# Kernel tuning notes

Hardware: AMD Instinct MI355X
Metric: run time of the kernel (lower is better)

The kernel has to match this reference:

```python
import jax, jax.numpy as jnp
import numpy as np

BATCH = 512
HIDDEN_DIM = 4096
NUM_CODES = 32
CODE_DIM = 64
CODEBOOK_SIZE = 1024


def _lsa_single(cost):
    """Rectangular Hungarian (Jonker-Volgenant shortest augmenting path).
    cost: [n, m] with n <= m. Returns, for each row, the assigned column,
    minimizing total cost (matches scipy.optimize.linear_sum_assignment)."""
    n, m = cost.shape
    u = np.zeros(n + 1)
    v = np.zeros(m + 1)
    p = np.zeros(m + 1, dtype=np.int64)  # p[j]: row matched to col j (1-based); 0 = free
    for i in range(1, n + 1):
        p[0] = i
        j0 = 0
        minv = np.full(m + 1, np.inf)
        way = np.zeros(m + 1, dtype=np.int64)
        used = np.zeros(m + 1, dtype=bool)
        while True:
            used[j0] = True
            i0 = p[j0]
            free = ~used
            free[0] = False
            jfree = np.nonzero(free)[0]
            cur = cost[i0 - 1, jfree - 1] - u[i0] - v[jfree]
            upd = cur < minv[jfree]
            minv[jfree[upd]] = cur[upd]
            way[jfree[upd]] = j0
            k = jfree[np.argmin(minv[jfree])]
            delta = minv[k]
            u[p[used]] += delta
            v[used] -= delta
            minv[free] -= delta
            j0 = k
            if p[j0] == 0:
                break
        while j0 != 0:  # augment along the path
            j1 = way[j0]
            p[j0] = p[j1]
            j0 = j1
    ans = np.empty(n, dtype=np.int64)
    for j in range(1, m + 1):
        if p[j] > 0:
            ans[p[j] - 1] = j - 1
    return ans


def _lsa_batch(costs):
    costs = np.asarray(costs, dtype=np.float64)
    return np.stack([_lsa_single(c) for c in costs]).astype(np.int32)


def setup_inputs() -> dict:
    key = jax.random.key(0)
    ks = jax.random.split(key, 4)
    return {
        "x": jax.random.normal(ks[0], (BATCH, HIDDEN_DIM), jnp.float32),
        "codebook": jax.random.normal(ks[1], (CODEBOOK_SIZE, CODE_DIM), jnp.float32),
        "enc_w": jax.random.normal(ks[2], (NUM_CODES * CODE_DIM, HIDDEN_DIM), jnp.float32) * 0.02,
        "enc_b": jnp.zeros((NUM_CODES * CODE_DIM,), jnp.float32),
        "dec_w": jax.random.normal(ks[3], (HIDDEN_DIM, NUM_CODES * CODE_DIM), jnp.float32) * 0.02,
        "dec_b": jnp.zeros((HIDDEN_DIM,), jnp.float32),
    }


def reference(x, codebook, enc_w, enc_b, dec_w, dec_b):
    bs = x.shape[0]
    # encoder (torch Linear: y = x @ W.T + b)
    e = (x @ enc_w.T + enc_b).reshape(bs, NUM_CODES, CODE_DIM)
    ef = e.reshape(-1, CODE_DIM)  # [bs*num_codes, code_dim]
    # pairwise Euclidean distances to codebook entries [bs*num_codes, codebook_size]
    d2 = (jnp.sum(ef * ef, axis=1, keepdims=True)
          + jnp.sum(codebook * codebook, axis=1)
          - 2.0 * (ef @ codebook.T))
    dist = jnp.sqrt(jnp.maximum(d2, 0.0)).reshape(bs, NUM_CODES, CODEBOOK_SIZE)
    # per-sample Hungarian assignment (original uses scipy on CPU; sqrt is
    # monotone so the optimal assignment is identical)
    indices = jax.pure_callback(
        _lsa_batch,
        jax.ShapeDtypeStruct((bs, NUM_CODES), jnp.int32),
        jax.lax.stop_gradient(dist),
    )
    flat_idx = indices.reshape(-1)  # matches torch's concatenated flat indices
    q = codebook[flat_idx].reshape(bs, NUM_CODES, CODE_DIM)
    # straight-through estimator
    q_st = e + jax.lax.stop_gradient(q - e)
    r = q_st.reshape(bs, NUM_CODES * CODE_DIM) @ dec_w.T + dec_b
    return (r, q, e, flat_idx)
```

## Files before the change

kernel.cpp:

```cpp
#include <hip/hip_runtime.h>
#include <hip/hip_bf16.h>
#include <stdint.h>

#define BATCH 512
#define HID   4096
#define NC    32
#define CD    64
#define CB    1024
#define NCD   2048

typedef unsigned short u16;
typedef unsigned int   u32;
typedef __attribute__((ext_vector_type(8))) short short8;
typedef __attribute__((ext_vector_type(4))) float f32x4;

#define WAVE_SYNC()  asm volatile("s_waitcnt lgkmcnt(0)" ::: "memory")
#define SCHED_FENCE() __builtin_amdgcn_sched_barrier(0)

__device__ inline u16 bf16_rne(float f) {
  u32 u = __builtin_bit_cast(u32, f);
  u32 r = u + 0x7FFFu + ((u >> 16) & 1u);
  return (u16)(r >> 16);
}
__device__ inline float bf16_f32(u16 h) {
  u32 u = ((u32)h) << 16;
  return __builtin_bit_cast(float, u);
}
__device__ inline void split3(float a, u16& h1, u16& h2, u16& h3) {
  h1 = bf16_rne(a);
  float r1 = a - bf16_f32(h1);
  h2 = bf16_rne(r1);
  float r2 = r1 - bf16_f32(h2);
  h3 = bf16_rne(r2);
}
__device__ inline f32x4 mfma16(short8 a, short8 b, f32x4 c) {
  return __builtin_amdgcn_mfma_f32_16x16x32_bf16(a, b, c, 0, 0, 0);
}
__device__ inline void gload_lds16(const u16* g, u16* l) {
  __builtin_amdgcn_global_load_lds(
      (const __attribute__((address_space(1))) u32*)(const void*)g,
      (__attribute__((address_space(3))) u32*)(void*)l, 16, 0, 0);
}

union H8 { u16 h[8]; short8 v; };

template<int K>
__global__ __launch_bounds__(256) void conv_split3(
    const float* __restrict__ src, u16* __restrict__ d1,
    u16* __restrict__ d2, u16* __restrict__ d3) {
  const int t = threadIdx.x;
  const int g = blockIdx.x * 4 + (t >> 6);
  const int l = t & 63;
  const int n  = (g / (K / 32)) * 16 + (l & 15);
  const int k0 = (g % (K / 32)) * 32 + (l >> 4) * 8;
  const float* s = src + (size_t)n * K + k0;
  H8 o1, o2, o3;
#pragma unroll
  for (int i = 0; i < 8; ++i) split3(s[i], o1.h[i], o2.h[i], o3.h[i]);
  size_t off = (size_t)g * 512 + l * 8;
  *(short8*)(d1 + off) = o1.v;
  *(short8*)(d2 + off) = o2.v;
  *(short8*)(d3 + off) = o3.v;
}

template<int K>
__global__ __launch_bounds__(256) void conv_split1(
    const float* __restrict__ src, u16* __restrict__ d1) {
  const int t = threadIdx.x;
  const int g = blockIdx.x * 4 + (t >> 6);
  const int l = t & 63;
  const int n  = (g / (K / 32)) * 16 + (l & 15);
  const int k0 = (g % (K / 32)) * 32 + (l >> 4) * 8;
  const float* s = src + (size_t)n * K + k0;
  H8 o1;
#pragma unroll
  for (int i = 0; i < 8; ++i) o1.h[i] = bf16_rne(s[i]);
  *(short8*)(d1 + (size_t)g * 512 + l * 8) = o1.v;
}

__global__ __launch_bounds__(512) void k1_gemm(
    const float* __restrict__ A,
    const u16* __restrict__ B1, const u16* __restrict__ B2,
    const u16* __restrict__ B3, float* __restrict__ part) {
  __shared__ u16 As[3][8][64][8];
  __shared__ u16 Bs[3][8][64][8];
  const int t = threadIdx.x;
  const int wid = t >> 6, lane = t & 63;
  const int wrow = wid >> 2, wcol = wid & 3;
  const int bm = blockIdx.x * 128;
  const int bn = blockIdx.y * 128;
  const int kz = blockIdx.z;
  const int kbase = kz * 1024;
  const int arow = t >> 2;
  const int akc  = t & 3;
  const float* aptr = A + (size_t)(bm + arow) * HID + kbase + akc * 8;
  const int arf = arow >> 4, all_ = (akc << 4) | (arow & 15);
  const size_t nf0 = (size_t)((bn >> 4) + wid);

  f32x4 acc[4][2];
#pragma unroll
  for (int r = 0; r < 4; ++r)
#pragma unroll
    for (int c = 0; c < 2; ++c) acc[r][c] = (f32x4)0.f;

  for (int ks = 0; ks < 32; ++ks) {
    float v[8];
    *(f32x4*)&v[0] = *(const f32x4*)(aptr + ks * 32);
    *(f32x4*)&v[4] = *(const f32x4*)(aptr + ks * 32 + 4);
    {
      size_t gb = (nf0 * 128 + (size_t)((kbase >> 5) + ks)) * 512 + lane * 8;
      gload_lds16(B1 + gb, &Bs[0][wid][0][0]);
      gload_lds16(B2 + gb, &Bs[1][wid][0][0]);
      gload_lds16(B3 + gb, &Bs[2][wid][0][0]);
    }
    {
      H8 s1, s2, s3;
#pragma unroll
      for (int i = 0; i < 8; ++i) split3(v[i], s1.h[i], s2.h[i], s3.h[i]);
      *(short8*)&As[0][arf][all_][0] = s1.v;
      *(short8*)&As[1][arf][all_][0] = s2.v;
      *(short8*)&As[2][arf][all_][0] = s3.v;
    }
    __syncthreads();
    short8 a0[4], a1[4], a2[4], b0[2], b1[2], b2[2];
#pragma unroll
    for (int r = 0; r < 4; ++r) {
      a0[r] = *(const short8*)&As[0][wrow * 4 + r][lane][0];
      a1[r] = *(const short8*)&As[1][wrow * 4 + r][lane][0];
      a2[r] = *(const short8*)&As[2][wrow * 4 + r][lane][0];
    }
#pragma unroll
    for (int c = 0; c < 2; ++c) {
      b0[c] = *(const short8*)&Bs[0][wcol * 2 + c][lane][0];
      b1[c] = *(const short8*)&Bs[1][wcol * 2 + c][lane][0];
      b2[c] = *(const short8*)&Bs[2][wcol * 2 + c][lane][0];
    }
#pragma unroll
    for (int r = 0; r < 4; ++r)
#pragma unroll
      for (int c = 0; c < 2; ++c) {
        f32x4 d = acc[r][c];
        d = mfma16(a0[r], b0[c], d);
        d = mfma16(a0[r], b1[c], d);
        d = mfma16(a1[r], b0[c], d);
        d = mfma16(a1[r], b1[c], d);
        d = mfma16(a0[r], b2[c], d);
        d = mfma16(a2[r], b0[c], d);
        acc[r][c] = d;
      }
    __syncthreads();
  }
  float* P = part + (size_t)kz * BATCH * NCD;
#pragma unroll
  for (int r = 0; r < 4; ++r)
#pragma unroll
    for (int c = 0; c < 2; ++c) {
      int row = bm + wrow * 64 + r * 16 + (lane >> 4) * 4;
      int col = bn + wcol * 32 + c * 16 + (lane & 15);
#pragma unroll
      for (int i = 0; i < 4; ++i)
        P[(size_t)(row + i) * NCD + col] = acc[r][c][i];
    }
}

__global__ __launch_bounds__(256) void k_reduce_bias(
    const float* __restrict__ part, const float* __restrict__ bias,
    float* __restrict__ e) {
  size_t o = ((size_t)blockIdx.x * 256 + threadIdx.x) * 4;
  int n = (int)(o & (NCD - 1));
  f32x4 s = *(const f32x4*)(part + o);
  s += *(const f32x4*)(part + (size_t)1 * BATCH * NCD + o);
  s += *(const f32x4*)(part + (size_t)2 * BATCH * NCD + o);
  s += *(const f32x4*)(part + (size_t)3 * BATCH * NCD + o);
  s += *(const f32x4*)(bias + n);
  *(f32x4*)(e + o) = s;
}

__global__ __launch_bounds__(512) void k3_gemm(
    const u16* __restrict__ Ab, const u16* __restrict__ Bb,
    const float* __restrict__ bias, float* __restrict__ C) {
  __shared__ u16 As[4][64][8];
  __shared__ u16 Bs[8][64][8];
  const int t = threadIdx.x;
  const int wid = t >> 6, lane = t & 63;
  const int wrow = wid >> 2, wcol = wid & 3;
  const int bm = blockIdx.x * 64, bn = blockIdx.y * 128;
  f32x4 acc[2][2];
#pragma unroll
  for (int r = 0; r < 2; ++r)
#pragma unroll
    for (int c = 0; c < 2; ++c) acc[r][c] = (f32x4)0.f;

  for (int ks = 0; ks < 64; ++ks) {
    {
      size_t gb = (((size_t)(bn >> 4) + wid) * 64 + ks) * 512 + lane * 8;
      gload_lds16(Bb + gb, &Bs[wid][0][0]);
      if (wid < 4) {
        size_t ga = (((size_t)(bm >> 4) + wid) * 64 + ks) * 512 + lane * 8;
        gload_lds16(Ab + ga, &As[wid][0][0]);
      }
    }
    __syncthreads();
    short8 a[2], b[2];
#pragma unroll
    for (int r = 0; r < 2; ++r) a[r] = *(const short8*)&As[wrow * 2 + r][lane][0];
#pragma unroll
    for (int c = 0; c < 2; ++c) b[c] = *(const short8*)&Bs[wcol * 2 + c][lane][0];
#pragma unroll
    for (int r = 0; r < 2; ++r)
#pragma unroll
      for (int c = 0; c < 2; ++c) acc[r][c] = mfma16(a[r], b[c], acc[r][c]);
    __syncthreads();
  }
#pragma unroll
  for (int r = 0; r < 2; ++r)
#pragma unroll
    for (int c = 0; c < 2; ++c) {
      int row = bm + wrow * 32 + r * 16 + (lane >> 4) * 4;
      int col = bn + wcol * 32 + c * 16 + (lane & 15);
      float bb = bias[col];
#pragma unroll
      for (int i = 0; i < 4; ++i)
        C[(size_t)(row + i) * HID + col] = acc[r][c][i] + bb;
    }
}

__global__ __launch_bounds__(256) void k_cost(
    const float* __restrict__ e_glob, const float* __restrict__ codebook,
    float* __restrict__ cost) {
  __shared__ float es[64][68];
  __shared__ float cs[64][68];
  __shared__ float enorm[64], cnorm[64];
  const int t = threadIdx.x;
  const int r0 = blockIdx.x * 64;
  const int c0 = blockIdx.y * 256;
  const int tx = t & 15, ty = t >> 4;
  {
    int row = t & 63, kq = t >> 6;
    const float* src = e_glob + (size_t)(r0 + row) * 64 + kq * 16;
#pragma unroll
    for (int i = 0; i < 4; ++i) {
      float4 v = *(const float4*)(src + i * 4);
      int kk = kq * 16 + i * 4;
      es[kk + 0][row] = v.x; es[kk + 1][row] = v.y;
      es[kk + 2][row] = v.z; es[kk + 3][row] = v.w;
    }
  }
  __syncthreads();
  if (t < 64) {
    float s = 0.f;
    for (int kk = 0; kk < 64; ++kk) { float x = es[kk][t]; s = fmaf(x, x, s); }
    enorm[t] = s;
  }
  for (int sub = 0; sub < 4; ++sub) {
    __syncthreads();
    {
      int col = t & 63, kq = t >> 6;
      const float* src = codebook + (size_t)(c0 + sub * 64 + col) * 64 + kq * 16;
#pragma unroll
      for (int i = 0; i < 4; ++i) {
        float4 v = *(const float4*)(src + i * 4);
        int kk = kq * 16 + i * 4;
        cs[kk + 0][col] = v.x; cs[kk + 1][col] = v.y;
        cs[kk + 2][col] = v.z; cs[kk + 3][col] = v.w;
      }
    }
    __syncthreads();
    if (t < 64) {
      float s = 0.f;
      for (int kk = 0; kk < 64; ++kk) { float x = cs[kk][t]; s = fmaf(x, x, s); }
      cnorm[t] = s;
    }
    __syncthreads();
    float dot[4][4] = {};
#pragma unroll 8
    for (int kk = 0; kk < 64; ++kk) {
      float4 a4 = *(const float4*)&es[kk][ty * 4];
      float4 b4 = *(const float4*)&cs[kk][tx * 4];
      float a_[4] = {a4.x, a4.y, a4.z, a4.w};
      float b_[4] = {b4.x, b4.y, b4.z, b4.w};
#pragma unroll
      for (int i = 0; i < 4; ++i)
#pragma unroll
        for (int j = 0; j < 4; ++j)
          dot[i][j] = fmaf(a_[i], b_[j], dot[i][j]);
    }
#pragma unroll
    for (int i = 0; i < 4; ++i) {
      int r = ty * 4 + i;
      float en = enorm[r];
      float4 o;
      o.x = sqrtf(fmaxf(en + cnorm[tx * 4 + 0] - 2.f * dot[i][0], 0.f));
      o.y = sqrtf(fmaxf(en + cnorm[tx * 4 + 1] - 2.f * dot[i][1], 0.f));
      o.z = sqrtf(fmaxf(en + cnorm[tx * 4 + 2] - 2.f * dot[i][2], 0.f));
      o.w = sqrtf(fmaxf(en + cnorm[tx * 4 + 3] - 2.f * dot[i][3], 0.f));
      *(float4*)&cost[(size_t)(r0 + r) * CB + c0 + sub * 64 + tx * 4] = o;
    }
  }
}

__global__ __launch_bounds__(64) void k_assign(
    const float* __restrict__ cost_g, const float* __restrict__ codebook,
    float* __restrict__ q_out, float* __restrict__ idx_out) {
  __shared__ int idxl[32];
  const int lane = threadIdx.x;
  const int s = blockIdx.x;
  const float* __restrict__ cost = cost_g + (size_t)s * NC * CB;

  double v_[16], minv_[16];
  u32 way_[16], pm_[16];
  double u_val = 0.0;
#pragma unroll
  for (int r = 0; r < 16; ++r) { v_[r] = 0.0; pm_[r] = 0; }

  float pf[16];
#pragma unroll
  for (int r = 0; r < 16; ++r) pf[r] = cost[r * 64 + lane];

  for (int i = 1; i <= NC; ++i) {
#pragma unroll
    for (int r = 0; r < 16; ++r) minv_[r] = 1e300;
    u32 col_used = 0;
    unsigned long long rowmask = 0ull;
    int j0 = 0;
    int i0 = i;
    int first = 1;
    for (int guard = 0; guard < 1056; ++guard) {
      rowmask |= (1ull << i0);
      const double ui0 = __shfl(u_val, i0);
      float cc[16];
      if (first) {
#pragma unroll
        for (int r = 0; r < 16; ++r) cc[r] = pf[r];
        if (i < NC) {
#pragma unroll
          for (int r = 0; r < 16; ++r)
            pf[r] = cost[(size_t)i * CB + r * 64 + lane];
        }
        first = 0;
      } else {
        const float* crow = cost + (size_t)(i0 - 1) * CB;
#pragma unroll
        for (int r = 0; r < 16; ++r) cc[r] = crow[r * 64 + lane];
      }
      double bv = 1e301; int bj = 1 << 20;
#pragma unroll
      for (int r = 0; r < 16; ++r) {
        const int j = 1 + lane + r * 64;
        if (!((col_used >> r) & 1u)) {
          double cur = (double)cc[r] - ui0 - v_[r];
          if (cur < minv_[r]) { minv_[r] = cur; way_[r] = (u32)j0; }
          if (minv_[r] < bv) { bv = minv_[r]; bj = j; }
        }
      }
#pragma unroll
      for (int off = 1; off < 64; off <<= 1) {
        double ov = __shfl_xor(bv, off);
        int oj = __shfl_xor(bj, off);
        if (ov < bv || (ov == bv && oj < bj)) { bv = ov; bj = oj; }
      }
      const double delta = bv;
      const int k = bj;
      if ((rowmask >> lane) & 1ull) u_val += delta;
#pragma unroll
      for (int r = 0; r < 16; ++r) {
        const int j = 1 + lane + r * 64;
        if ((col_used >> r) & 1u) v_[r] -= delta;
        else {
          minv_[r] -= delta;
          if (j == k) col_used |= (1u << r);
        }
      }
      const int rk = (k - 1) >> 6, kl = (k - 1) & 63;
      u32 sel = 0;
#pragma unroll
      for (int r = 0; r < 16; ++r) if (r == rk) sel = pm_[r];
      const int pmk = __shfl((int)sel, kl);
      j0 = k;
      if (pmk == 0) break;
      i0 = pmk;
    }
    int jj = j0;
    while (jj != 0) {
      const int rj = (jj - 1) >> 6, lj = (jj - 1) & 63;
      u32 wsel = 0;
#pragma unroll
      for (int r = 0; r < 16; ++r) if (r == rj) wsel = way_[r];
      const int j1 = __shfl((int)wsel, lj);
      int newpm;
      if (j1 == 0) newpm = i;
      else {
        const int r1 = (j1 - 1) >> 6, l1 = (j1 - 1) & 63;
        u32 psel = 0;
#pragma unroll
        for (int r = 0; r < 16; ++r) if (r == r1) psel = pm_[r];
        newpm = __shfl((int)psel, l1);
      }
#pragma unroll
      for (int r = 0; r < 16; ++r)
        if (lane == lj && r == rj) pm_[r] = (u32)newpm;
      jj = j1;
    }
  }

#pragma unroll
  for (int r = 0; r < 16; ++r)
    if (pm_[r] > 0) idxl[pm_[r] - 1] = lane + r * 64;
  WAVE_SYNC(); SCHED_FENCE();
  if (lane < NC) idx_out[(size_t)s * NC + lane] = (float)idxl[lane];
#pragma unroll
  for (int p = 0; p < 8; ++p) {
    int vi = p * 64 + lane;
    int r = vi >> 4, c4 = vi & 15;
    int ci = idxl[r];
    float4 qv = *(const float4*)&codebook[(size_t)ci * 64 + c4 * 4];
    *(float4*)&q_out[(size_t)s * NCD + r * 64 + c4 * 4] = qv;
  }
}

extern "C" void kernel_launch(void* const* d_in, const int* in_sizes, int n_in,
                              void* d_out, int out_size, void* d_ws, size_t ws_size,
                              hipStream_t stream) {
  (void)in_sizes; (void)n_in; (void)out_size; (void)ws_size;
  const float* x        = (const float*)d_in[0];
  const float* codebook = (const float*)d_in[1];
  const float* enc_w    = (const float*)d_in[2];
  const float* enc_b    = (const float*)d_in[3];
  const float* dec_w    = (const float*)d_in[4];
  const float* dec_b    = (const float*)d_in[5];

  float* out = (float*)d_out;
  float* r_out   = out;
  float* q_out   = out + 2097152;
  float* e_out   = out + 2097152 + 1048576;
  float* idx_out = out + 2097152 + 2097152;

  char* ws = (char*)d_ws;
  u16* B1 = (u16*)ws;
  u16* B2 = (u16*)(ws + (16u << 20));
  u16* B3 = (u16*)(ws + (32u << 20));
  float* part = (float*)(ws + (48u << 20));
  float* cost_ws = (float*)ws;
  u16* qb  = (u16*)ws;
  u16* dwb = (u16*)(ws + (2u << 20));

  conv_split3<HID><<<4096, 256, 0, stream>>>(enc_w, B1, B2, B3);
  k1_gemm<<<dim3(4, 16, 4), 512, 0, stream>>>(x, B1, B2, B3, part);
  k_reduce_bias<<<1024, 256, 0, stream>>>(part, enc_b, e_out);
  k_cost<<<dim3(16384 / 64, CB / 256), 256, 0, stream>>>(e_out, codebook, cost_ws);
  k_assign<<<BATCH, 64, 0, stream>>>(cost_ws, codebook, q_out, idx_out);
  conv_split1<NCD><<<4096, 256, 0, stream>>>(dec_w, dwb);
  conv_split1<NCD><<<512, 256, 0, stream>>>(q_out, qb);
  k3_gemm<<<dim3(8, 32), 512, 0, stream>>>(qb, dwb, dec_b, r_out);
}
```

Measured before the change: 250.7 us.

## Double-buffer encoder GEMM LDS with swizzle; pack way/match arrays in assignment kernel

The encoder GEMM now double-buffers its A and B LDS tiles. The next k-slice's global loads are issued before the current MFMAs, and its bf16 split and store come after them, so there is one barrier per step instead of two. The A tile gets an XOR swizzle to reduce LDS bank conflicts. The Hungarian kernel packs the way and match arrays into one u32 per column and declares one-wave occupancy, to save registers on the serial path. LDS use doubles, and the packing adds shift and mask work on every access.

After: 232.2 us. -7.3%, faster.

```diff
diff --git a/kernel.cpp b/kernel.cpp
--- a/kernel.cpp
+++ b/kernel.cpp
@@ -82,8 +82,8 @@
     const float* __restrict__ A,
     const u16* __restrict__ B1, const u16* __restrict__ B2,
     const u16* __restrict__ B3, float* __restrict__ part) {
-  __shared__ u16 As[3][8][64][8];
-  __shared__ u16 Bs[3][8][64][8];
+  __shared__ u16 As[2][3][8][64][8];
+  __shared__ u16 Bs[2][3][8][64][8];
   const int t = threadIdx.x;
   const int wid = t >> 6, lane = t & 63;
   const int wrow = wid >> 2, wcol = wid & 3;
@@ -94,7 +94,10 @@
   const int arow = t >> 2;
   const int akc  = t & 3;
   const float* aptr = A + (size_t)(bm + arow) * HID + kbase + akc * 8;
-  const int arf = arow >> 4, all_ = (akc << 4) | (arow & 15);
+  const int arf = arow >> 4;
+  const int p_w = (akc << 4) | (arow & 15);
+  const int s_w = p_w ^ ((p_w >> 4) & 3);
+  const int s_r = lane ^ ((lane >> 4) & 3);
   const size_t nf0 = (size_t)((bn >> 4) + wid);
 
   f32x4 acc[4][2];
@@ -103,37 +106,46 @@
 #pragma unroll
     for (int c = 0; c < 2; ++c) acc[r][c] = (f32x4)0.f;
 
+  {
+    float va[8];
+    *(f32x4*)&va[0] = *(const f32x4*)(aptr);
+    *(f32x4*)&va[4] = *(const f32x4*)(aptr + 4);
+    size_t gb = (nf0 * 128 + (size_t)(kbase >> 5)) * 512 + lane * 8;
+    gload_lds16(B1 + gb, &Bs[0][0][wid][0][0]);
+    gload_lds16(B2 + gb, &Bs[0][1][wid][0][0]);
+    gload_lds16(B3 + gb, &Bs[0][2][wid][0][0]);
+    H8 s1, s2, s3;
+#pragma unroll
+    for (int i = 0; i < 8; ++i) split3(va[i], s1.h[i], s2.h[i], s3.h[i]);
+    *(short8*)&As[0][0][arf][s_w][0] = s1.v;
+    *(short8*)&As[0][1][arf][s_w][0] = s2.v;
+    *(short8*)&As[0][2][arf][s_w][0] = s3.v;
+  }
+  __syncthreads();
+
   for (int ks = 0; ks < 32; ++ks) {
-    float v[8];
-    *(f32x4*)&v[0] = *(const f32x4*)(aptr + ks * 32);
-    *(f32x4*)&v[4] = *(const f32x4*)(aptr + ks * 32 + 4);
-    {
-      size_t gb = (nf0 * 128 + (size_t)((kbase >> 5) + ks)) * 512 + lane * 8;
-      gload_lds16(B1 + gb, &Bs[0][wid][0][0]);
-      gload_lds16(B2 + gb, &Bs[1][wid][0][0]);
-      gload_lds16(B3 + gb, &Bs[2][wid][0][0]);
-    }
-    {
-      H8 s1, s2, s3;
-#pragma unroll
-      for (int i = 0; i < 8; ++i) split3(v[i], s1.h[i], s2.h[i], s3.h[i]);
-      *(short8*)&As[0][arf][all_][0] = s1.v;
-      *(short8*)&As[1][arf][all_][0] = s2.v;
-      *(short8*)&As[2][arf][all_][0] = s3.v;
-    }
-    __syncthreads();
+    const int cur = ks & 1, nxt = cur ^ 1;
+    float vb[8];
+    if (ks < 31) {
+      *(f32x4*)&vb[0] = *(const f32x4*)(aptr + (ks + 1) * 32);
+      *(f32x4*)&vb[4] = *(const f32x4*)(aptr + (ks + 1) * 32 + 4);
+      size_t gb = (nf0 * 128 + (size_t)((kbase >> 5) + ks + 1)) * 512 + lane * 8;
+      gload_lds16(B1 + gb, &Bs[nxt][0][wid][0][0]);
+      gload_lds16(B2 + gb, &Bs[nxt][1][wid][0][0]);
+      gload_lds16(B3 + gb, &Bs[nxt][2][wid][0][0]);
+    }
     short8 a0[4], a1[4], a2[4], b0[2], b1[2], b2[2];
 #pragma unroll
     for (int r = 0; r < 4; ++r) {
-      a0[r] = *(const short8*)&As[0][wrow * 4 + r][lane][0];
-      a1[r] = *(const short8*)&As[1][wrow * 4 + r][lane][0];
-      a2[r] = *(const short8*)&As[2][wrow * 4 + r][lane][0];
+      a0[r] = *(const short8*)&As[cur][0][wrow * 4 + r][s_r][0];
+      a1[r] = *(const short8*)&As[cur][1][wrow * 4 + r][s_r][0];
+      a2[r] = *(const short8*)&As[cur][2][wrow * 4 + r][s_r][0];
     }
 #pragma unroll
     for (int c = 0; c < 2; ++c) {
-      b0[c] = *(const short8*)&Bs[0][wcol * 2 + c][lane][0];
-      b1[c] = *(const short8*)&Bs[1][wcol * 2 + c][lane][0];
-      b2[c] = *(const short8*)&Bs[2][wcol * 2 + c][lane][0];
+      b0[c] = *(const short8*)&Bs[cur][0][wcol * 2 + c][lane][0];
+      b1[c] = *(const short8*)&Bs[cur][1][wcol * 2 + c][lane][0];
+      b2[c] = *(const short8*)&Bs[cur][2][wcol * 2 + c][lane][0];
     }
 #pragma unroll
     for (int r = 0; r < 4; ++r)
@@ -148,6 +160,14 @@
         d = mfma16(a2[r], b0[c], d);
         acc[r][c] = d;
       }
+    if (ks < 31) {
+      H8 s1, s2, s3;
+#pragma unroll
+      for (int i = 0; i < 8; ++i) split3(vb[i], s1.h[i], s2.h[i], s3.h[i]);
+      *(short8*)&As[nxt][0][arf][s_w][0] = s1.v;
+      *(short8*)&As[nxt][1][arf][s_w][0] = s2.v;
+      *(short8*)&As[nxt][2][arf][s_w][0] = s3.v;
+    }
     __syncthreads();
   }
   float* P = part + (size_t)kz * BATCH * NCD;
@@ -299,7 +319,7 @@
   }
 }
 
-__global__ __launch_bounds__(64) void k_assign(
+__global__ __launch_bounds__(64, 1) void k_assign(
     const float* __restrict__ cost_g, const float* __restrict__ codebook,
     float* __restrict__ q_out, float* __restrict__ idx_out) {
   __shared__ int idxl[32];
@@ -308,10 +328,10 @@
   const float* __restrict__ cost = cost_g + (size_t)s * NC * CB;
 
   double v_[16], minv_[16];
-  u32 way_[16], pm_[16];
+  u32 wp_[16];
   double u_val = 0.0;
 #pragma unroll
-  for (int r = 0; r < 16; ++r) { v_[r] = 0.0; pm_[r] = 0; }
+  for (int r = 0; r < 16; ++r) { v_[r] = 0.0; wp_[r] = 0; }
 
   float pf[16];
 #pragma unroll
@@ -349,7 +369,7 @@
         const int j = 1 + lane + r * 64;
         if (!((col_used >> r) & 1u)) {
           double cur = (double)cc[r] - ui0 - v_[r];
-          if (cur < minv_[r]) { minv_[r] = cur; way_[r] = (u32)j0; }
+          if (cur < minv_[r]) { minv_[r] = cur; wp_[r] = (wp_[r] & 0xFFFF0000u) | (u32)j0; }
           if (minv_[r] < bv) { bv = minv_[r]; bj = j; }
         }
       }
@@ -374,8 +394,8 @@
       const int rk = (k - 1) >> 6, kl = (k - 1) & 63;
       u32 sel = 0;
 #pragma unroll
-      for (int r = 0; r < 16; ++r) if (r == rk) sel = pm_[r];
-      const int pmk = __shfl((int)sel, kl);
+      for (int r = 0; r < 16; ++r) if (r == rk) sel = wp_[r];
+      const int pmk = ((u32)__shfl((int)sel, kl)) >> 16;
       j0 = k;
       if (pmk == 0) break;
       i0 = pmk;
@@ -385,27 +405,29 @@
       const int rj = (jj - 1) >> 6, lj = (jj - 1) & 63;
       u32 wsel = 0;
 #pragma unroll
-      for (int r = 0; r < 16; ++r) if (r == rj) wsel = way_[r];
-      const int j1 = __shfl((int)wsel, lj);
+      for (int r = 0; r < 16; ++r) if (r == rj) wsel = wp_[r];
+      const int j1 = ((u32)__shfl((int)wsel, lj)) & 0xFFFFu;
       int newpm;
       if (j1 == 0) newpm = i;
       else {
         const int r1 = (j1 - 1) >> 6, l1 = (j1 - 1) & 63;
         u32 psel = 0;
 #pragma unroll
-        for (int r = 0; r < 16; ++r) if (r == r1) psel = pm_[r];
-        newpm = __shfl((int)psel, l1);
+        for (int r = 0; r < 16; ++r) if (r == r1) psel = wp_[r];
+        newpm = ((u32)__shfl((int)psel, l1)) >> 16;
       }
 #pragma unroll
       for (int r = 0; r < 16; ++r)
-        if (lane == lj && r == rj) pm_[r] = (u32)newpm;
+        if (lane == lj && r == rj) wp_[r] = (wp_[r] & 0xFFFFu) | ((u32)newpm << 16);
       jj = j1;
     }
   }
 
 #pragma unroll
-  for (int r = 0; r < 16; ++r)
-    if (pm_[r] > 0) idxl[pm_[r] - 1] = lane + r * 64;
+  for (int r = 0; r < 16; ++r) {
+    const u32 pm = wp_[r] >> 16;
+    if (pm > 0) idxl[pm - 1] = lane + r * 64;
+  }
   WAVE_SYNC(); SCHED_FENCE();
   if (lane < NC) idx_out[(size_t)s * NC + lane] = (float)idxl[lane];
 #pragma unroll
```
